# Kernel tuning notes

Hardware: AMD Instinct MI355X
Metric: run time of the kernel (lower is better)

Reference implementation:

```python
import jax, jax.numpy as jnp
import numpy as np

N = 100000      # num nodes
E = 1600000     # num edges (avg degree 16)
IN = 128        # in_channels
OUT = 64        # out_channels
HID = 2 * OUT   # conv1 output width = 2*out_channels


def setup_inputs() -> dict:
    key = jax.random.key(0)
    k0, k1, k2, k3 = jax.random.split(key, 4)
    x = jax.random.uniform(k0, (N, IN), dtype=jnp.float32)
    edge_index = jax.random.randint(k1, (2, E), 0, N, dtype=jnp.int32)
    # GCNConv weights (glorot-style uniform), biases zero-init as in PyG
    s1 = float(np.sqrt(6.0 / (IN + HID)))
    W1 = jax.random.uniform(k2, (IN, HID), minval=-s1, maxval=s1, dtype=jnp.float32)
    b1 = jnp.zeros((HID,), dtype=jnp.float32)
    s2 = float(np.sqrt(6.0 / (HID + OUT)))
    W2 = jax.random.uniform(k3, (HID, OUT), minval=-s2, maxval=s2, dtype=jnp.float32)
    b2 = jnp.zeros((OUT,), dtype=jnp.float32)
    return {"x": x, "edge_index": edge_index, "W1": W1, "b1": b1, "W2": W2, "b2": b2}


def gcn_conv(x, W, b, src, dst, n):
    """PyG GCNConv: self-loops + symmetric deg^-1/2 normalization + scatter-add."""
    h = x @ W                                   # [n, d_out] dense transform first
    loops = jnp.arange(n, dtype=src.dtype)
    s = jnp.concatenate([src, loops])           # [E+n] sources (with self-loops)
    d = jnp.concatenate([dst, loops])           # [E+n] destinations
    deg = jax.ops.segment_sum(jnp.ones_like(s, dtype=h.dtype), d, num_segments=n)
    dinv = jnp.where(deg > 0, jax.lax.rsqrt(deg), 0.0)
    norm = dinv[s] * dinv[d]                    # [E+n]
    # gather -> scale -> scatter-add aggregation
    out = jax.ops.segment_sum(h[s] * norm[:, None], d, num_segments=n)
    return out + b


def reference(x, edge_index, W1, b1, W2, b2):
    src, dst = edge_index[0], edge_index[1]
    n = x.shape[0]
    h = jax.nn.relu(gcn_conv(x, W1, b1, src, dst, n))
    return gcn_conv(h, W2, b2, src, dst, n)
```

## Files before the change

kernel.cpp:

```cpp
#include <hip/hip_runtime.h>

#define IN_C  128
#define HID_C 128
#define OUT_C 64
#define NPB      128
#define NPB_SH   7
#define NPB_MASK 127
#define MAXB     2048
#define CAP      6144
#define B1_CHUNK 8192

__device__ __forceinline__ unsigned short f2bf(float f) {
    unsigned u = __float_as_uint(f);
    unsigned r = (u + 0x7FFFu + ((u >> 16) & 1u)) >> 16;
    return (unsigned short)r;
}
__device__ __forceinline__ float bf_lo(unsigned u) { return __uint_as_float(u << 16); }
__device__ __forceinline__ float bf_hi(unsigned u) { return __uint_as_float(u & 0xFFFF0000u); }


__global__ __launch_bounds__(256) void hist_kernel(const int* __restrict__ dst,
                                                   int* __restrict__ bhist,
                                                   int E, int B) {
    __shared__ int lh[MAXB];
    int t = threadIdx.x;
    int e0 = blockIdx.x * B1_CHUNK;
    int nE = min(B1_CHUNK, E - e0);
    if (B <= MAXB) {
        for (int i = t; i < B; i += 256) lh[i] = 0;
        __syncthreads();
        for (int i = t; i < nE; i += 256) atomicAdd(&lh[dst[e0 + i] >> NPB_SH], 1);
        __syncthreads();
        for (int i = t; i < B; i += 256)
            if (lh[i]) atomicAdd(&bhist[i], lh[i]);
    } else {
        for (int i = t; i < nE; i += 256) atomicAdd(&bhist[dst[e0 + i] >> NPB_SH], 1);
    }
}

__global__ __launch_bounds__(1024) void scan_bucket_kernel(const int* __restrict__ bhist,
                                                           int* __restrict__ bbase,
                                                           int* __restrict__ bcur, int B) {
    __shared__ int sums[1024];
    int t = threadIdx.x;
    int chunk = (B + 1023) >> 10;
    int beg = t * chunk, end = min(beg + chunk, B);
    int s = 0;
    for (int i = beg; i < end; ++i) s += bhist[i];
    sums[t] = s;
    __syncthreads();
    for (int off = 1; off < 1024; off <<= 1) {
        int v = (t >= off) ? sums[t - off] : 0;
        __syncthreads();
        sums[t] += v;
        __syncthreads();
    }
    int run = (t == 0) ? 0 : sums[t - 1];
    for (int i = beg; i < end; ++i) {
        bbase[i] = run; bcur[i] = run;
        run += bhist[i];
    }
    if (t == 1023) bbase[B] = sums[1023];
}

__global__ __launch_bounds__(256) void bucket_kernel(const int* __restrict__ src,
                                                     const int* __restrict__ dst,
                                                     int* __restrict__ bcur,
                                                     int* __restrict__ ebuf,
                                                     int E, int B) {
    __shared__ int hist[MAXB];
    __shared__ int runb[MAXB];
    int t = threadIdx.x;
    int e0 = blockIdx.x * B1_CHUNK;
    int nE = min(B1_CHUNK, E - e0);
    if (B <= MAXB) {
        for (int i = t; i < B; i += 256) hist[i] = 0;
        __syncthreads();
        for (int i = t; i < nE; i += 256) atomicAdd(&hist[dst[e0 + i] >> NPB_SH], 1);
        __syncthreads();
        for (int i = t; i < B; i += 256) {
            int c = hist[i];
            runb[i] = c ? atomicAdd(&bcur[i], c) : 0;
            hist[i] = 0;
        }
        __syncthreads();
        for (int i = t; i < nE; i += 256) {
            int d = dst[e0 + i], s = src[e0 + i];
            int b = d >> NPB_SH;
            int off2 = atomicAdd(&hist[b], 1);
            ebuf[runb[b] + off2] = (s << NPB_SH) | (d & NPB_MASK);
        }
    } else {
        for (int i = t; i < nE; i += 256) {
            int d = dst[e0 + i], s = src[e0 + i];
            int pos = atomicAdd(&bcur[d >> NPB_SH], 1);
            ebuf[pos] = (s << NPB_SH) | (d & NPB_MASK);
        }
    }
}

__global__ __launch_bounds__(256) void csr_kernel(const int* __restrict__ ebuf,
                                                  const int* __restrict__ bbase,
                                                  int* __restrict__ col,
                                                  int* __restrict__ rowptr,
                                                  float* __restrict__ dinv,
                                                  int N, int E) {
    __shared__ int sorted[CAP];
    __shared__ int lhist[NPB];
    __shared__ int lpre[NPB + 1];
    int b = blockIdx.x;
    int t = threadIdx.x;
    int base = bbase[b], size = bbase[b + 1] - base;
    int node_base = b << NPB_SH;
    int nn = min(NPB, N - node_base);

    if (t < NPB) lhist[t] = 0;
    __syncthreads();
    for (int i = t; i < size; i += 256) atomicAdd(&lhist[ebuf[base + i] & NPB_MASK], 1);
    __syncthreads();
    if (t < NPB) lpre[t + 1] = lhist[t];
    if (t == 0) lpre[0] = 0;
    __syncthreads();
    for (int off = 1; off < NPB; off <<= 1) {
        int v = (t >= off && t < NPB) ? lpre[t + 1 - off] : 0;
        __syncthreads();
        if (t < NPB) lpre[t + 1] += v;
        __syncthreads();
    }
    if (t < nn) {
        rowptr[node_base + t] = base + lpre[t];
        dinv[node_base + t] = rsqrtf((float)(lhist[t] + 1));
    }
    if (node_base + nn == N && t == 0) rowptr[N] = base + size;
    if (t < NPB) lhist[t] = lpre[t];
    __syncthreads();
    if (size <= CAP) {
        for (int i = t; i < size; i += 256) {
            int entry = ebuf[base + i];
            int slot = atomicAdd(&lhist[entry & NPB_MASK], 1);
            sorted[slot] = entry >> NPB_SH;
        }
        __syncthreads();
        for (int i = t; i < size; i += 256) col[base + i] = sorted[i];
    } else {
        for (int i = t; i < size; i += 256) {
            int entry = ebuf[base + i];
            int slot = atomicAdd(&lhist[entry & NPB_MASK], 1);
            col[base + slot] = entry >> NPB_SH;
        }
    }
}


__global__ __launch_bounds__(256) void mm_kernel(
    const float* __restrict__ X, const float* __restrict__ W,
    const float* __restrict__ dinv, unsigned short* __restrict__ Hs,
    int n, int outc) {
    __shared__ float xs[64 * 128];
    __shared__ float ws[128 * 64];
    int t = threadIdx.x;
    int row0 = blockIdx.x * 64;
    int c0 = blockIdx.y * 64;

    for (int i = t; i < (64 * 128) / 4; i += 256) {
        int idx = i * 4;
        int r = idx >> 7, k = idx & 127;
        int row = row0 + r;
        float4 v = make_float4(0.f, 0.f, 0.f, 0.f);
        if (row < n) v = *(const float4*)&X[(size_t)row * 128 + k];
        *(float4*)&xs[idx] = v;
    }
    for (int i = t; i < (128 * 64) / 4; i += 256) {
        int idx = i * 4;
        int k = idx >> 6, c = idx & 63;
        *(float4*)&ws[idx] = *(const float4*)&W[(size_t)k * outc + c0 + c];
    }
    __syncthreads();

    int tc = t & 15, tr = t >> 4;
    int r0 = tr * 4, cc = tc * 4;
    float acc[4][4] = {};
    for (int k = 0; k < 128; k += 4) {
        float4 xv[4], wv[4];
#pragma unroll
        for (int i = 0; i < 4; ++i) xv[i] = *(const float4*)&xs[(r0 + i) * 128 + k];
#pragma unroll
        for (int j = 0; j < 4; ++j) wv[j] = *(const float4*)&ws[(k + j) * 64 + cc];
#pragma unroll
        for (int i = 0; i < 4; ++i) {
            acc[i][0] += xv[i].x * wv[0].x + xv[i].y * wv[1].x + xv[i].z * wv[2].x + xv[i].w * wv[3].x;
            acc[i][1] += xv[i].x * wv[0].y + xv[i].y * wv[1].y + xv[i].z * wv[2].y + xv[i].w * wv[3].y;
            acc[i][2] += xv[i].x * wv[0].z + xv[i].y * wv[1].z + xv[i].z * wv[2].z + xv[i].w * wv[3].z;
            acc[i][3] += xv[i].x * wv[0].w + xv[i].y * wv[1].w + xv[i].z * wv[2].w + xv[i].w * wv[3].w;
        }
    }
#pragma unroll
    for (int i = 0; i < 4; ++i) {
        int row = row0 + r0 + i;
        if (row < n) {
            float s = dinv[row];
            ushort4 o;
            o.x = f2bf(s * acc[i][0]);
            o.y = f2bf(s * acc[i][1]);
            o.z = f2bf(s * acc[i][2]);
            o.w = f2bf(s * acc[i][3]);
            *(ushort4*)&Hs[(size_t)row * outc + c0 + cc] = o;
        }
    }
}


template<int C>
__global__ __launch_bounds__(256) void agg_kernel(
    const unsigned short* __restrict__ Hs, const float* __restrict__ bias,
    const float* __restrict__ dinv, const int* __restrict__ rowptr,
    const int* __restrict__ col, float* __restrict__ out, int n, int relu) {
    constexpr int LPR = C / 8;
    constexpr int SLOTS = 64 / LPR;
    int d = (blockIdx.x * 256 + threadIdx.x) >> 6;
    if (d >= n) return;
    int lane = threadIdx.x & 63;
    int cl = lane & (LPR - 1);
    int slot = lane / LPR;

    float acc[8] = {0.f, 0.f, 0.f, 0.f, 0.f, 0.f, 0.f, 0.f};
    int beg = rowptr[d], end = rowptr[d + 1];

    for (int j = beg; j < end; j += 2 * SLOTS) {
        int i0 = j + slot, i1 = j + SLOTS + slot;
        uint4 v0 = make_uint4(0, 0, 0, 0), v1 = make_uint4(0, 0, 0, 0);
        if (i0 < end) v0 = *((const uint4*)(Hs + (size_t)col[i0] * C) + cl);
        if (i1 < end) v1 = *((const uint4*)(Hs + (size_t)col[i1] * C) + cl);
        acc[0] += bf_lo(v0.x) + bf_lo(v1.x);
        acc[1] += bf_hi(v0.x) + bf_hi(v1.x);
        acc[2] += bf_lo(v0.y) + bf_lo(v1.y);
        acc[3] += bf_hi(v0.y) + bf_hi(v1.y);
        acc[4] += bf_lo(v0.z) + bf_lo(v1.z);
        acc[5] += bf_hi(v0.z) + bf_hi(v1.z);
        acc[6] += bf_lo(v0.w) + bf_lo(v1.w);
        acc[7] += bf_hi(v0.w) + bf_hi(v1.w);
    }
#pragma unroll
    for (int m = LPR; m < 64; m <<= 1) {
#pragma unroll
        for (int k = 0; k < 8; ++k) acc[k] += __shfl_xor(acc[k], m, 64);
    }
    uint4 sv = *((const uint4*)(Hs + (size_t)d * C) + cl);
    acc[0] += bf_lo(sv.x); acc[1] += bf_hi(sv.x);
    acc[2] += bf_lo(sv.y); acc[3] += bf_hi(sv.y);
    acc[4] += bf_lo(sv.z); acc[5] += bf_hi(sv.z);
    acc[6] += bf_lo(sv.w); acc[7] += bf_hi(sv.w);

    float dv = dinv[d];
    float4 b0 = *((const float4*)bias + cl * 2);
    float4 b1 = *((const float4*)bias + cl * 2 + 1);
    float r[8];
    r[0] = dv * acc[0] + b0.x; r[1] = dv * acc[1] + b0.y;
    r[2] = dv * acc[2] + b0.z; r[3] = dv * acc[3] + b0.w;
    r[4] = dv * acc[4] + b1.x; r[5] = dv * acc[5] + b1.y;
    r[6] = dv * acc[6] + b1.z; r[7] = dv * acc[7] + b1.w;
    if (relu) {
#pragma unroll
        for (int k = 0; k < 8; ++k) r[k] = fmaxf(r[k], 0.f);
    }
    if (slot == 0) {
        float* o = out + (size_t)d * C + cl * 8;
        *(float4*)o = make_float4(r[0], r[1], r[2], r[3]);
        *(float4*)(o + 4) = make_float4(r[4], r[5], r[6], r[7]);
    }
}


extern "C" void kernel_launch(void* const* d_in, const int* in_sizes, int n_in,
                              void* d_out, int out_size, void* d_ws, size_t ws_size,
                              hipStream_t stream) {
    const float* x  = (const float*)d_in[0];
    const int*   ei = (const int*)d_in[1];
    const float* W1 = (const float*)d_in[2];
    const float* b1 = (const float*)d_in[3];
    const float* W2 = (const float*)d_in[4];
    const float* b2 = (const float*)d_in[5];
    float* out = (float*)d_out;

    int N = in_sizes[0] / IN_C;
    int E = in_sizes[1] / 2;
    const int* src = ei;
    const int* dst = ei + E;
    int B = (N + NPB - 1) >> NPB_SH;

    char* ws = (char*)d_ws;
    size_t off = 0;
    int*   bhist  = (int*)(ws + off);   off += (size_t)B * 4;
    int*   bbase  = (int*)(ws + off);   off += (size_t)(B + 1) * 4;
    int*   bcur   = (int*)(ws + off);   off += (size_t)B * 4;
    float* dinv   = (float*)(ws + off); off += (size_t)N * 4;
    int*   rowptr = (int*)(ws + off);   off += (size_t)(N + 1) * 4;
    off = (off + 15) & ~(size_t)15;
    int*   ebuf   = (int*)(ws + off);   off += (size_t)E * 4;
    int*   col    = (int*)(ws + off);   off += (size_t)E * 4;
    off = (off + 15) & ~(size_t)15;
    unsigned short* H1 = (unsigned short*)(ws + off); off += (size_t)N * HID_C * 2;
    off = (off + 15) & ~(size_t)15;
    float* AG1    = (float*)(ws + off); off += (size_t)N * HID_C * 4;
    unsigned short* H2 = H1;

    hipMemsetAsync(bhist, 0, (size_t)B * 4, stream);

    int nblk = (E + B1_CHUNK - 1) / B1_CHUNK;
    hist_kernel<<<nblk, 256, 0, stream>>>(dst, bhist, E, B);
    scan_bucket_kernel<<<1, 1024, 0, stream>>>(bhist, bbase, bcur, B);
    bucket_kernel<<<nblk, 256, 0, stream>>>(src, dst, bcur, ebuf, E, B);
    csr_kernel<<<B, 256, 0, stream>>>(ebuf, bbase, col, rowptr, dinv, N, E);

    dim3 g1((N + 63) / 64, HID_C / 64);
    mm_kernel<<<g1, 256, 0, stream>>>(x, W1, dinv, H1, N, HID_C);
    agg_kernel<HID_C><<<(N + 3) / 4, 256, 0, stream>>>(H1, b1, dinv, rowptr, col, AG1, N, 1);

    dim3 g2((N + 63) / 64, OUT_C / 64);
    mm_kernel<<<g2, 256, 0, stream>>>(AG1, W2, dinv, H2, N, OUT_C);
    agg_kernel<OUT_C><<<(N + 3) / 4, 256, 0, stream>>>(H2, b2, dinv, rowptr, col, out, N, 0);
}
```

Measured before the change: 408.0 us.

## Use bf16 MFMA for dense transforms and store hidden activations as bf16

Replaces the scalar-FMA shared-memory GEMM with a kernel built on mfma_f32_16x16x32_bf16. It converts W to a transposed bf16 tile in LDS and reads X rows directly from global memory. The first aggregation now writes its ReLU output as bf16, which halves the intermediate write and the second GEMM's read. The cost is extra rounding of inputs and intermediates to bf16, plus scalar 2-byte stores in the GEMM epilogue.

```diff
diff --git a/kernel.cpp b/kernel.cpp
--- a/kernel.cpp
+++ b/kernel.cpp
@@ -9,6 +9,9 @@
 #define MAXB     2048
 #define CAP      6144
 #define B1_CHUNK 8192
+
+typedef __attribute__((ext_vector_type(8))) short short8;
+typedef __attribute__((ext_vector_type(4))) float f32x4;
 
 __device__ __forceinline__ unsigned short f2bf(float f) {
     unsigned u = __float_as_uint(f);
@@ -152,69 +155,78 @@
 }
 
 
-__global__ __launch_bounds__(256) void mm_kernel(
-    const float* __restrict__ X, const float* __restrict__ W,
-    const float* __restrict__ dinv, unsigned short* __restrict__ Hs,
-    int n, int outc) {
-    __shared__ float xs[64 * 128];
-    __shared__ float ws[128 * 64];
-    int t = threadIdx.x;
-    int row0 = blockIdx.x * 64;
-    int c0 = blockIdx.y * 64;
-
-    for (int i = t; i < (64 * 128) / 4; i += 256) {
+template<int C, typename InT>
+__global__ __launch_bounds__(256) void mm_mfma_kernel(
+    const InT* __restrict__ X, const float* __restrict__ W,
+    const float* __restrict__ dinv, unsigned short* __restrict__ Hs, int n) {
+    constexpr int LD = 136;
+    __shared__ unsigned short Wt[C][LD];
+    int t = threadIdx.x;
+
+    for (int i = t; i < (128 * C) / 4; i += 256) {
         int idx = i * 4;
-        int r = idx >> 7, k = idx & 127;
-        int row = row0 + r;
-        float4 v = make_float4(0.f, 0.f, 0.f, 0.f);
-        if (row < n) v = *(const float4*)&X[(size_t)row * 128 + k];
-        *(float4*)&xs[idx] = v;
-    }
-    for (int i = t; i < (128 * 64) / 4; i += 256) {
-        int idx = i * 4;
-        int k = idx >> 6, c = idx & 63;
-        *(float4*)&ws[idx] = *(const float4*)&W[(size_t)k * outc + c0 + c];
-    }
-    __syncthreads();
-
-    int tc = t & 15, tr = t >> 4;
-    int r0 = tr * 4, cc = tc * 4;
-    float acc[4][4] = {};
-    for (int k = 0; k < 128; k += 4) {
-        float4 xv[4], wv[4];
-#pragma unroll
-        for (int i = 0; i < 4; ++i) xv[i] = *(const float4*)&xs[(r0 + i) * 128 + k];
-#pragma unroll
-        for (int j = 0; j < 4; ++j) wv[j] = *(const float4*)&ws[(k + j) * 64 + cc];
-#pragma unroll
-        for (int i = 0; i < 4; ++i) {
-            acc[i][0] += xv[i].x * wv[0].x + xv[i].y * wv[1].x + xv[i].z * wv[2].x + xv[i].w * wv[3].x;
-            acc[i][1] += xv[i].x * wv[0].y + xv[i].y * wv[1].y + xv[i].z * wv[2].y + xv[i].w * wv[3].y;
-            acc[i][2] += xv[i].x * wv[0].z + xv[i].y * wv[1].z + xv[i].z * wv[2].z + xv[i].w * wv[3].z;
-            acc[i][3] += xv[i].x * wv[0].w + xv[i].y * wv[1].w + xv[i].z * wv[2].w + xv[i].w * wv[3].w;
-        }
-    }
-#pragma unroll
-    for (int i = 0; i < 4; ++i) {
-        int row = row0 + r0 + i;
-        if (row < n) {
-            float s = dinv[row];
-            ushort4 o;
-            o.x = f2bf(s * acc[i][0]);
-            o.y = f2bf(s * acc[i][1]);
-            o.z = f2bf(s * acc[i][2]);
-            o.w = f2bf(s * acc[i][3]);
-            *(ushort4*)&Hs[(size_t)row * outc + c0 + cc] = o;
-        }
-    }
-}
-
-
-template<int C>
+        int k = idx / C, c = idx % C;
+        float4 wv = *(const float4*)&W[(size_t)k * C + c];
+        Wt[c + 0][k] = f2bf(wv.x);
+        Wt[c + 1][k] = f2bf(wv.y);
+        Wt[c + 2][k] = f2bf(wv.z);
+        Wt[c + 3][k] = f2bf(wv.w);
+    }
+    __syncthreads();
+
+    int w = t >> 6, lane = t & 63;
+    int m = lane & 15, quad = lane >> 4;
+    int row0 = blockIdx.x * 64 + w * 16;
+    int arow = min(row0 + m, n - 1);
+
+    constexpr int NT = C / 16;
+    f32x4 acc[NT];
+#pragma unroll
+    for (int ct = 0; ct < NT; ++ct) acc[ct] = (f32x4){0.f, 0.f, 0.f, 0.f};
+
+#pragma unroll
+    for (int kk = 0; kk < 4; ++kk) {
+        int k0 = kk * 32 + quad * 8;
+        short8 a;
+        if constexpr (sizeof(InT) == 4) {
+            const float* xp = (const float*)X + (size_t)arow * 128 + k0;
+            float4 f0 = *(const float4*)xp;
+            float4 f1 = *(const float4*)(xp + 4);
+            a[0] = (short)f2bf(f0.x); a[1] = (short)f2bf(f0.y);
+            a[2] = (short)f2bf(f0.z); a[3] = (short)f2bf(f0.w);
+            a[4] = (short)f2bf(f1.x); a[5] = (short)f2bf(f1.y);
+            a[6] = (short)f2bf(f1.z); a[7] = (short)f2bf(f1.w);
+        } else {
+            a = *(const short8*)((const unsigned short*)X + (size_t)arow * 128 + k0);
+        }
+#pragma unroll
+        for (int ct = 0; ct < NT; ++ct) {
+            short8 b = *(const short8*)&Wt[ct * 16 + m][k0];
+            acc[ct] = __builtin_amdgcn_mfma_f32_16x16x32_bf16(a, b, acc[ct], 0, 0, 0);
+        }
+    }
+
+    int qrow = row0 + quad * 4;
+    float dv[4];
+#pragma unroll
+    for (int r = 0; r < 4; ++r) dv[r] = (qrow + r < n) ? dinv[qrow + r] : 0.f;
+#pragma unroll
+    for (int ct = 0; ct < NT; ++ct) {
+        int c = ct * 16 + m;
+#pragma unroll
+        for (int r = 0; r < 4; ++r) {
+            int row = qrow + r;
+            if (row < n) Hs[(size_t)row * C + c] = f2bf(acc[ct][r] * dv[r]);
+        }
+    }
+}
+
+
+template<int C, bool BOUT>
 __global__ __launch_bounds__(256) void agg_kernel(
     const unsigned short* __restrict__ Hs, const float* __restrict__ bias,
     const float* __restrict__ dinv, const int* __restrict__ rowptr,
-    const int* __restrict__ col, float* __restrict__ out, int n, int relu) {
+    const int* __restrict__ col, void* __restrict__ outv, int n, int relu) {
     constexpr int LPR = C / 8;
     constexpr int SLOTS = 64 / LPR;
     int d = (blockIdx.x * 256 + threadIdx.x) >> 6;
@@ -241,9 +253,9 @@
         acc[7] += bf_hi(v0.w) + bf_hi(v1.w);
     }
 #pragma unroll
-    for (int m = LPR; m < 64; m <<= 1) {
-#pragma unroll
-        for (int k = 0; k < 8; ++k) acc[k] += __shfl_xor(acc[k], m, 64);
+    for (int mk = LPR; mk < 64; mk <<= 1) {
+#pragma unroll
+        for (int k = 0; k < 8; ++k) acc[k] += __shfl_xor(acc[k], mk, 64);
     }
     uint4 sv = *((const uint4*)(Hs + (size_t)d * C) + cl);
     acc[0] += bf_lo(sv.x); acc[1] += bf_hi(sv.x);
@@ -264,9 +276,18 @@
         for (int k = 0; k < 8; ++k) r[k] = fmaxf(r[k], 0.f);
     }
     if (slot == 0) {
-        float* o = out + (size_t)d * C + cl * 8;
-        *(float4*)o = make_float4(r[0], r[1], r[2], r[3]);
-        *(float4*)(o + 4) = make_float4(r[4], r[5], r[6], r[7]);
+        if constexpr (BOUT) {
+            uint4 o;
+            o.x = (unsigned)f2bf(r[0]) | ((unsigned)f2bf(r[1]) << 16);
+            o.y = (unsigned)f2bf(r[2]) | ((unsigned)f2bf(r[3]) << 16);
+            o.z = (unsigned)f2bf(r[4]) | ((unsigned)f2bf(r[5]) << 16);
+            o.w = (unsigned)f2bf(r[6]) | ((unsigned)f2bf(r[7]) << 16);
+            *(uint4*)((unsigned short*)outv + (size_t)d * C + cl * 8) = o;
+        } else {
+            float* o = (float*)outv + (size_t)d * C + cl * 8;
+            *(float4*)o = make_float4(r[0], r[1], r[2], r[3]);
+            *(float4*)(o + 4) = make_float4(r[4], r[5], r[6], r[7]);
+        }
     }
 }
 
@@ -299,9 +320,9 @@
     int*   ebuf   = (int*)(ws + off);   off += (size_t)E * 4;
     int*   col    = (int*)(ws + off);   off += (size_t)E * 4;
     off = (off + 15) & ~(size_t)15;
-    unsigned short* H1 = (unsigned short*)(ws + off); off += (size_t)N * HID_C * 2;
+    unsigned short* H1  = (unsigned short*)(ws + off); off += (size_t)N * HID_C * 2;
     off = (off + 15) & ~(size_t)15;
-    float* AG1    = (float*)(ws + off); off += (size_t)N * HID_C * 4;
+    unsigned short* AG1 = (unsigned short*)(ws + off); off += (size_t)N * HID_C * 2;
     unsigned short* H2 = H1;
 
     hipMemsetAsync(bhist, 0, (size_t)B * 4, stream);
@@ -312,11 +333,10 @@
     bucket_kernel<<<nblk, 256, 0, stream>>>(src, dst, bcur, ebuf, E, B);
     csr_kernel<<<B, 256, 0, stream>>>(ebuf, bbase, col, rowptr, dinv, N, E);
 
-    dim3 g1((N + 63) / 64, HID_C / 64);
-    mm_kernel<<<g1, 256, 0, stream>>>(x, W1, dinv, H1, N, HID_C);
-    agg_kernel<HID_C><<<(N + 3) / 4, 256, 0, stream>>>(H1, b1, dinv, rowptr, col, AG1, N, 1);
-
-    dim3 g2((N + 63) / 64, OUT_C / 64);
-    mm_kernel<<<g2, 256, 0, stream>>>(AG1, W2, dinv, H2, N, OUT_C);
-    agg_kernel<OUT_C><<<(N + 3) / 4, 256, 0, stream>>>(H2, b2, dinv, rowptr, col, out, N, 0);
-}
+    int mblk = (N + 63) / 64;
+    mm_mfma_kernel<HID_C, float><<<mblk, 256, 0, stream>>>(x, W1, dinv, H1, N);
+    agg_kernel<HID_C, true><<<(N + 3) / 4, 256, 0, stream>>>(H1, b1, dinv, rowptr, col, AG1, N, 1);
+
+    mm_mfma_kernel<OUT_C, unsigned short><<<mblk, 256, 0, stream>>>(AG1, W2, dinv, H2, N);
+    agg_kernel<OUT_C, false><<<(N + 3) / 4, 256, 0, stream>>>(H2, b2, dinv, rowptr, col, out, N, 0);
+}
```

Result: faster. 340.7 us (-16.5%).
